# Optimization experiments

Hardware: AMD Instinct MI355X
Metric: run time of the kernel (lower is better)

## Reference

```python
import jax, jax.numpy as jnp
import numpy as np

D_MODEL = 1024
TEMPERATURE = 1.0

def setup_inputs() -> dict:
    key = jax.random.key(0)
    ks = jax.random.split(key, 9)
    B, NQ, NK, D = 4, 2048, 2048, D_MODEL
    s = 1.0 / np.sqrt(D)
    return {
        "Q": jax.random.normal(ks[0], (B, NQ, D), jnp.float32),
        "K": jax.random.normal(ks[1], (B, NK, D), jnp.float32),
        "V": jax.random.normal(ks[2], (B, NK, D), jnp.float32),
        "Wq": jax.random.normal(ks[3], (D, D), jnp.float32) * s,
        "bq": jax.random.normal(ks[4], (D,), jnp.float32) * 0.01,
        "Wk": jax.random.normal(ks[5], (D, D), jnp.float32) * s,
        "bk": jax.random.normal(ks[6], (D,), jnp.float32) * 0.01,
        "Wv": jax.random.normal(ks[7], (D, D), jnp.float32) * s,
        "bv": jax.random.normal(ks[8], (D,), jnp.float32) * 0.01,
    }

def reference(Q, K, V, Wq, bq, Wk, bk, Wv, bv):
    # torch nn.Linear: y = x @ W.T + b
    Qp = Q @ Wq.T + bq  # [B, NQ, D]
    Kp = K @ Wk.T + bk  # [B, NK, D]
    Vp = V @ Wv.T + bv  # [B, NK, D]

    # use_kl=True branch, vectorized:
    # kl[b,i,j] = D_KL(softmax(Kp[b,j]) || softmax(Qp[b,i]))
    #           = sum_d pK*(log pK - log pQ) = -H(pK_j) - pK_j . log pQ_i
    logpQ = jax.nn.log_softmax(Qp, axis=-1)  # [B, NQ, D]
    logpK = jax.nn.log_softmax(Kp, axis=-1)  # [B, NK, D]
    pK = jnp.exp(logpK)
    neg_ent_K = jnp.sum(pK * logpK, axis=-1)            # [B, NK], = -H(pK)
    cross = jnp.einsum('bjd,bid->bij', pK, logpQ)       # [B, NQ, NK]
    kl = neg_ent_K[:, None, :] - cross                  # [B, NQ, NK]
    scores = -kl / TEMPERATURE

    attn = jax.nn.softmax(scores, axis=-1)              # [B, NQ, NK]
    out = jnp.einsum('bij,bjd->bid', attn, Vp)          # [B, NQ, D]
    return out, attn
```

## Files before the change

### kernel.cpp

```cpp
#include <hip/hip_runtime.h>
#include <math.h>

#define D_MODEL 1024
#define NQS 2048
#define NKS 2048
#define BATCH 4

typedef __attribute__((ext_vector_type(8))) short bf16x8;
typedef __attribute__((ext_vector_type(4))) float f32x4;

#define AS1 __attribute__((address_space(1)))
#define AS3 __attribute__((address_space(3)))

__device__ __forceinline__ unsigned short f2bf(float f) {
  unsigned u = __builtin_bit_cast(unsigned, f);
  u = (u + 0x7FFF + ((u >> 16) & 1)) >> 16;
  return (unsigned short)u;
}
__device__ __forceinline__ float bf2f(unsigned short s) {
  return __builtin_bit_cast(float, ((unsigned)s) << 16);
}

__global__ __launch_bounds__(256) void cvt_k(const float* __restrict__ src,
                                             short* __restrict__ dst, int n8)
{
  int i = blockIdx.x * 256 + threadIdx.x;
  if (i >= n8) return;
  const float4 a = *(const float4*)&src[(long)i * 8];
  const float4 b = *(const float4*)&src[(long)i * 8 + 4];
  bf16x8 o;
  o[0] = (short)f2bf(a.x); o[1] = (short)f2bf(a.y);
  o[2] = (short)f2bf(a.z); o[3] = (short)f2bf(a.w);
  o[4] = (short)f2bf(b.x); o[5] = (short)f2bf(b.y);
  o[6] = (short)f2bf(b.z); o[7] = (short)f2bf(b.w);
  *(bf16x8*)&dst[(long)i * 8] = o;
}

__global__ __launch_bounds__(256, 2) void mfma_abt_k(
    const short* __restrict__ A, const short* __restrict__ B,
    const float* __restrict__ bias, float bscale,
    float* __restrict__ Cf, short* __restrict__ Cbf,
    int N, int K, long sA, long sB, long sC, long sBias)
{
  __shared__ short As[128 * 32];
  __shared__ short Bs[128 * 32];
  const int bz = blockIdx.z;
  const short* Ab = A + (long)bz * sA;
  const short* Bb = B + (long)bz * sB;
  const int gm = blockIdx.y * 128, gn = blockIdx.x * 128;
  const int t = threadIdx.x;
  const int lane = t & 63, w = t >> 6;
  const int wm = w >> 1, wn = w & 1;

  const int srow = lane >> 2, sq = lane & 3;
  const short* ga0 = Ab + (long)(gm + w * 32 + srow) * K + sq * 8;
  const short* ga1 = Ab + (long)(gm + w * 32 + 16 + srow) * K + sq * 8;
  const short* gb0 = Bb + (long)(gn + w * 32 + srow) * K + sq * 8;
  const short* gb1 = Bb + (long)(gn + w * 32 + 16 + srow) * K + sq * 8;
  short* la0 = As + (w * 2 + 0) * 512;
  short* la1 = As + (w * 2 + 1) * 512;
  short* lb0 = Bs + (w * 2 + 0) * 512;
  short* lb1 = Bs + (w * 2 + 1) * 512;

  const int frow = lane & 15, fq = lane >> 4;

  f32x4 acc[4][4] = {};

  for (int k0 = 0; k0 < K; k0 += 32) {
    __builtin_amdgcn_global_load_lds((const AS1 void*)(ga0 + k0),
                                     (AS3 void*)la0, 16, 0, 0);
    __builtin_amdgcn_global_load_lds((const AS1 void*)(ga1 + k0),
                                     (AS3 void*)la1, 16, 0, 0);
    __builtin_amdgcn_global_load_lds((const AS1 void*)(gb0 + k0),
                                     (AS3 void*)lb0, 16, 0, 0);
    __builtin_amdgcn_global_load_lds((const AS1 void*)(gb1 + k0),
                                     (AS3 void*)lb1, 16, 0, 0);
    __syncthreads();
    bf16x8 af[4], bfm[4];
#pragma unroll
    for (int mi = 0; mi < 4; ++mi)
      af[mi] = *(const bf16x8*)&As[(wm * 64 + mi * 16 + frow) * 32 + fq * 8];
#pragma unroll
    for (int ni = 0; ni < 4; ++ni)
      bfm[ni] = *(const bf16x8*)&Bs[(wn * 64 + ni * 16 + frow) * 32 + fq * 8];
#pragma unroll
    for (int mi = 0; mi < 4; ++mi)
#pragma unroll
      for (int ni = 0; ni < 4; ++ni)
        acc[mi][ni] = __builtin_amdgcn_mfma_f32_16x16x32_bf16(
            af[mi], bfm[ni], acc[mi][ni], 0, 0, 0);
    __syncthreads();
  }

  float bb[4];
#pragma unroll
  for (int ni = 0; ni < 4; ++ni)
    bb[ni] = bias ? bias[(long)bz * sBias + gn + wn * 64 + ni * 16 + frow] * bscale
                  : 0.f;

#pragma unroll
  for (int mi = 0; mi < 4; ++mi) {
#pragma unroll
    for (int r = 0; r < 4; ++r) {
      const long row = gm + wm * 64 + mi * 16 + fq * 4 + r;
#pragma unroll
      for (int ni = 0; ni < 4; ++ni) {
        const long col = gn + wn * 64 + ni * 16 + frow;
        float v = acc[mi][ni][r] + bb[ni];
        if (Cf) Cf[(long)bz * sC + row * N + col] = v;
        else    Cbf[(long)bz * sC + row * N + col] = (short)f2bf(v);
      }
    }
  }
}

__global__ __launch_bounds__(256) void kstats_k(short* __restrict__ KP,
                                                float* __restrict__ negent)
{
  __shared__ float red[4];
  const long row = blockIdx.x;
  short* x = KP + row * (long)D_MODEL;
  const int t = threadIdx.x;
  short4 raw = *(const short4*)&x[t * 4];
  float v0 = bf2f((unsigned short)raw.x), v1 = bf2f((unsigned short)raw.y);
  float v2 = bf2f((unsigned short)raw.z), v3 = bf2f((unsigned short)raw.w);
  float m = fmaxf(fmaxf(v0, v1), fmaxf(v2, v3));
  for (int o = 32; o; o >>= 1) m = fmaxf(m, __shfl_xor(m, o));
  if ((t & 63) == 0) red[t >> 6] = m;
  __syncthreads();
  m = fmaxf(fmaxf(red[0], red[1]), fmaxf(red[2], red[3]));
  __syncthreads();
  float e0 = expf(v0 - m), e1 = expf(v1 - m), e2 = expf(v2 - m),
        e3 = expf(v3 - m);
  float s = e0 + e1 + e2 + e3;
  for (int o = 32; o; o >>= 1) s += __shfl_xor(s, o);
  if ((t & 63) == 0) red[t >> 6] = s;
  __syncthreads();
  s = red[0] + red[1] + red[2] + red[3];
  __syncthreads();
  const float inv = 1.0f / s;
  const float lse = m + logf(s);
  float p0 = e0 * inv, p1 = e1 * inv, p2 = e2 * inv, p3 = e3 * inv;
  float ne = p0 * (v0 - lse) + p1 * (v1 - lse) + p2 * (v2 - lse) +
             p3 * (v3 - lse);
  for (int o = 32; o; o >>= 1) ne += __shfl_xor(ne, o);
  if ((t & 63) == 0) red[t >> 6] = ne;
  __syncthreads();
  if (t == 0) negent[row] = red[0] + red[1] + red[2] + red[3];
  short4 pw;
  pw.x = (short)f2bf(p0); pw.y = (short)f2bf(p1);
  pw.z = (short)f2bf(p2); pw.w = (short)f2bf(p3);
  *(short4*)&x[t * 4] = pw;
}

__global__ __launch_bounds__(256) void asoftmax_k(float* __restrict__ S,
                                                  short* __restrict__ Sbf)
{
  __shared__ float red[4];
  const long row = blockIdx.x;
  float* x = S + row * (long)NKS;
  short* y = Sbf + row * (long)NKS;
  const int t = threadIdx.x;
  float4 v0 = *(const float4*)&x[t * 4];
  float4 v1 = *(const float4*)&x[1024 + t * 4];
  float m = fmaxf(fmaxf(fmaxf(v0.x, v0.y), fmaxf(v0.z, v0.w)),
                  fmaxf(fmaxf(v1.x, v1.y), fmaxf(v1.z, v1.w)));
  for (int o = 32; o; o >>= 1) m = fmaxf(m, __shfl_xor(m, o));
  if ((t & 63) == 0) red[t >> 6] = m;
  __syncthreads();
  m = fmaxf(fmaxf(red[0], red[1]), fmaxf(red[2], red[3]));
  __syncthreads();
  float4 e0 = {expf(v0.x - m), expf(v0.y - m), expf(v0.z - m), expf(v0.w - m)};
  float4 e1 = {expf(v1.x - m), expf(v1.y - m), expf(v1.z - m), expf(v1.w - m)};
  float s = e0.x + e0.y + e0.z + e0.w + e1.x + e1.y + e1.z + e1.w;
  for (int o = 32; o; o >>= 1) s += __shfl_xor(s, o);
  if ((t & 63) == 0) red[t >> 6] = s;
  __syncthreads();
  s = red[0] + red[1] + red[2] + red[3];
  const float inv = 1.0f / s;
  float4 p0 = {e0.x * inv, e0.y * inv, e0.z * inv, e0.w * inv};
  float4 p1 = {e1.x * inv, e1.y * inv, e1.z * inv, e1.w * inv};
  *(float4*)&x[t * 4] = p0;
  *(float4*)&x[1024 + t * 4] = p1;
  short4 b0, b1;
  b0.x = (short)f2bf(p0.x); b0.y = (short)f2bf(p0.y);
  b0.z = (short)f2bf(p0.z); b0.w = (short)f2bf(p0.w);
  b1.x = (short)f2bf(p1.x); b1.y = (short)f2bf(p1.y);
  b1.z = (short)f2bf(p1.z); b1.w = (short)f2bf(p1.w);
  *(short4*)&y[t * 4] = b0;
  *(short4*)&y[1024 + t * 4] = b1;
}

__global__ __launch_bounds__(256) void transpose_k(const short* __restrict__ src,
                                                   short* __restrict__ dst)
{
  __shared__ short tile[64][68];
  const int j0 = blockIdx.x * 64;
  const int d0 = blockIdx.y * 64;
  const int t = threadIdx.x;
  const int r = t >> 2, c = t & 3;
#pragma unroll
  for (int i = 0; i < 4; ++i)
    *(short4*)&tile[r][c * 16 + i * 4] =
        *(const short4*)&src[(long)(j0 + r) * D_MODEL + d0 + c * 16 + i * 4];
  __syncthreads();
  const long b = j0 >> 11;
  const int jj = j0 & 2047;
#pragma unroll
  for (int i = 0; i < 4; ++i) {
    short4 o;
    o.x = tile[c * 16 + i * 4 + 0][r];
    o.y = tile[c * 16 + i * 4 + 1][r];
    o.z = tile[c * 16 + i * 4 + 2][r];
    o.w = tile[c * 16 + i * 4 + 3][r];
    *(short4*)&dst[b * ((long)D_MODEL * NKS) + (long)(d0 + r) * NKS + jj +
                   c * 16 + i * 4] = o;
  }
}

extern "C" void kernel_launch(void* const* d_in, const int* in_sizes, int n_in,
                              void* d_out, int out_size, void* d_ws,
                              size_t ws_size, hipStream_t stream)
{
  const float* Q = (const float*)d_in[0];
  const float* K = (const float*)d_in[1];
  const float* V = (const float*)d_in[2];
  const float* Wq = (const float*)d_in[3];
  const float* bq = (const float*)d_in[4];
  const float* Wk = (const float*)d_in[5];
  const float* bk = (const float*)d_in[6];
  const float* Wv = (const float*)d_in[7];
  const float* bv = (const float*)d_in[8];

  float* out = (float*)d_out;
  float* attn = out + (long)BATCH * NQS * D_MODEL;

  const long SZ = (long)BATCH * NQS * D_MODEL;
  short* ws = (short*)d_ws;
  short* Qbf = ws;
  short* Kbf = ws + SZ;
  short* Vbf = ws + 2 * SZ;
  short* Qp  = ws + 3 * SZ;
  short* pK  = ws + 4 * SZ;
  short* Vp  = ws + 5 * SZ;
  float* negent = (float*)(ws + 6 * SZ);
  short* attn_bf = ws;
  short* Vpt = ws + 2 * SZ;

  short* Wqb = (short*)attn;
  short* Wkb = Wqb + (long)D_MODEL * D_MODEL;
  short* Wvb = Wkb + (long)D_MODEL * D_MODEL;

  dim3 blk(256);
  const int n8x = (int)(SZ / 8);
  const int n8w = D_MODEL * D_MODEL / 8;

  cvt_k<<<dim3(n8x / 256), blk, 0, stream>>>(Q, Qbf, n8x);
  cvt_k<<<dim3(n8x / 256), blk, 0, stream>>>(K, Kbf, n8x);
  cvt_k<<<dim3(n8x / 256), blk, 0, stream>>>(V, Vbf, n8x);
  cvt_k<<<dim3(n8w / 256), blk, 0, stream>>>(Wq, Wqb, n8w);
  cvt_k<<<dim3(n8w / 256), blk, 0, stream>>>(Wk, Wkb, n8w);
  cvt_k<<<dim3(n8w / 256), blk, 0, stream>>>(Wv, Wvb, n8w);

  dim3 gp(D_MODEL / 128, (BATCH * NQS) / 128, 1);
  mfma_abt_k<<<gp, blk, 0, stream>>>(Qbf, Wqb, bq, 1.0f, nullptr, Qp,
                                     D_MODEL, D_MODEL, 0, 0, 0, 0);
  mfma_abt_k<<<gp, blk, 0, stream>>>(Kbf, Wkb, bk, 1.0f, nullptr, pK,
                                     D_MODEL, D_MODEL, 0, 0, 0, 0);
  mfma_abt_k<<<gp, blk, 0, stream>>>(Vbf, Wvb, bv, 1.0f, nullptr, Vp,
                                     D_MODEL, D_MODEL, 0, 0, 0, 0);

  kstats_k<<<dim3(BATCH * NKS), blk, 0, stream>>>(pK, negent);

  transpose_k<<<dim3((BATCH * NKS) / 64, D_MODEL / 64), blk, 0, stream>>>(Vp,
                                                                          Vpt);

  dim3 gs(NKS / 128, NQS / 128, BATCH);
  mfma_abt_k<<<gs, blk, 0, stream>>>(
      Qp, pK, negent, -1.0f, attn, nullptr, NKS, D_MODEL,
      (long)NQS * D_MODEL, (long)NKS * D_MODEL, (long)NQS * NKS, NKS);

  asoftmax_k<<<dim3(BATCH * NQS), blk, 0, stream>>>(attn, attn_bf);

  dim3 go(D_MODEL / 128, NQS / 128, BATCH);
  mfma_abt_k<<<go, blk, 0, stream>>>(
      attn_bf, Vpt, nullptr, 0.f, out, nullptr, D_MODEL, NKS,
      (long)NQS * NKS, (long)D_MODEL * NKS, (long)NQS * D_MODEL, 0);
}
```

Measured before the change: 430.8 us.

## Batch conversions and QKV projections into grouped launches, raise occupancy, use fast exp

```diff
diff --git a/kernel.cpp b/kernel.cpp
--- a/kernel.cpp
+++ b/kernel.cpp
@@ -21,9 +21,14 @@
   return __builtin_bit_cast(float, ((unsigned)s) << 16);
 }
 
-__global__ __launch_bounds__(256) void cvt_k(const float* __restrict__ src,
-                                             short* __restrict__ dst, int n8)
-{
+__global__ __launch_bounds__(256) void cvt3_k(
+    const float* __restrict__ s0, const float* __restrict__ s1,
+    const float* __restrict__ s2, short* __restrict__ d0,
+    short* __restrict__ d1, short* __restrict__ d2, int n8)
+{
+  const int z = blockIdx.z;
+  const float* src = z == 0 ? s0 : (z == 1 ? s1 : s2);
+  short* dst = z == 0 ? d0 : (z == 1 ? d1 : d2);
   int i = blockIdx.x * 256 + threadIdx.x;
   if (i >= n8) return;
   const float4 a = *(const float4*)&src[(long)i * 8];
@@ -36,17 +41,13 @@
   *(bf16x8*)&dst[(long)i * 8] = o;
 }
 
-__global__ __launch_bounds__(256, 2) void mfma_abt_k(
-    const short* __restrict__ A, const short* __restrict__ B,
-    const float* __restrict__ bias, float bscale,
-    float* __restrict__ Cf, short* __restrict__ Cbf,
-    int N, int K, long sA, long sB, long sC, long sBias)
+__device__ __forceinline__ void gemm_tile_body(
+    const short* __restrict__ Ab, const short* __restrict__ Bb,
+    const float* __restrict__ bias, float bscale, float* __restrict__ Cf,
+    short* __restrict__ Cbf, int N, int K)
 {
   __shared__ short As[128 * 32];
   __shared__ short Bs[128 * 32];
-  const int bz = blockIdx.z;
-  const short* Ab = A + (long)bz * sA;
-  const short* Bb = B + (long)bz * sB;
   const int gm = blockIdx.y * 128, gn = blockIdx.x * 128;
   const int t = threadIdx.x;
   const int lane = t & 63, w = t >> 6;
@@ -95,8 +96,7 @@
   float bb[4];
 #pragma unroll
   for (int ni = 0; ni < 4; ++ni)
-    bb[ni] = bias ? bias[(long)bz * sBias + gn + wn * 64 + ni * 16 + frow] * bscale
-                  : 0.f;
+    bb[ni] = bias ? bias[gn + wn * 64 + ni * 16 + frow] * bscale : 0.f;
 
 #pragma unroll
   for (int mi = 0; mi < 4; ++mi) {
@@ -107,11 +107,40 @@
       for (int ni = 0; ni < 4; ++ni) {
         const long col = gn + wn * 64 + ni * 16 + frow;
         float v = acc[mi][ni][r] + bb[ni];
-        if (Cf) Cf[(long)bz * sC + row * N + col] = v;
-        else    Cbf[(long)bz * sC + row * N + col] = (short)f2bf(v);
+        if (Cf) Cf[row * (long)N + col] = v;
+        else    Cbf[row * (long)N + col] = (short)f2bf(v);
       }
     }
   }
+}
+
+__global__ __launch_bounds__(256, 4) void mfma_abt_k(
+    const short* __restrict__ A, const short* __restrict__ B,
+    const float* __restrict__ bias, float bscale, float* __restrict__ Cf,
+    short* __restrict__ Cbf, int N, int K, long sA, long sB, long sC,
+    long sBias)
+{
+  const int bz = blockIdx.z;
+  gemm_tile_body(A + (long)bz * sA, B + (long)bz * sB,
+                 bias ? bias + (long)bz * sBias : nullptr, bscale,
+                 Cf ? Cf + (long)bz * sC : nullptr,
+                 Cbf ? Cbf + (long)bz * sC : nullptr, N, K);
+}
+
+__global__ __launch_bounds__(256, 4) void mfma_proj_k(
+    const short* __restrict__ Xq, const short* __restrict__ Xk,
+    const short* __restrict__ Xv, const short* __restrict__ Wq,
+    const short* __restrict__ Wk, const short* __restrict__ Wv,
+    const float* __restrict__ bq, const float* __restrict__ bk,
+    const float* __restrict__ bv, short* __restrict__ Oq,
+    short* __restrict__ Ok, short* __restrict__ Ov)
+{
+  const int z = blockIdx.z;
+  const short* X = z == 0 ? Xq : (z == 1 ? Xk : Xv);
+  const short* W = z == 0 ? Wq : (z == 1 ? Wk : Wv);
+  const float* bias = z == 0 ? bq : (z == 1 ? bk : bv);
+  short* O = z == 0 ? Oq : (z == 1 ? Ok : Ov);
+  gemm_tile_body(X, W, bias, 1.0f, nullptr, O, D_MODEL, D_MODEL);
 }
 
 __global__ __launch_bounds__(256) void kstats_k(short* __restrict__ KP,
@@ -130,8 +159,8 @@
   __syncthreads();
   m = fmaxf(fmaxf(red[0], red[1]), fmaxf(red[2], red[3]));
   __syncthreads();
-  float e0 = expf(v0 - m), e1 = expf(v1 - m), e2 = expf(v2 - m),
-        e3 = expf(v3 - m);
+  float e0 = __expf(v0 - m), e1 = __expf(v1 - m), e2 = __expf(v2 - m),
+        e3 = __expf(v3 - m);
   float s = e0 + e1 + e2 + e3;
   for (int o = 32; o; o >>= 1) s += __shfl_xor(s, o);
   if ((t & 63) == 0) red[t >> 6] = s;
@@ -139,7 +168,7 @@
   s = red[0] + red[1] + red[2] + red[3];
   __syncthreads();
   const float inv = 1.0f / s;
-  const float lse = m + logf(s);
+  const float lse = m + __logf(s);
   float p0 = e0 * inv, p1 = e1 * inv, p2 = e2 * inv, p3 = e3 * inv;
   float ne = p0 * (v0 - lse) + p1 * (v1 - lse) + p2 * (v2 - lse) +
              p3 * (v3 - lse);
@@ -170,8 +199,10 @@
   __syncthreads();
   m = fmaxf(fmaxf(red[0], red[1]), fmaxf(red[2], red[3]));
   __syncthreads();
-  float4 e0 = {expf(v0.x - m), expf(v0.y - m), expf(v0.z - m), expf(v0.w - m)};
-  float4 e1 = {expf(v1.x - m), expf(v1.y - m), expf(v1.z - m), expf(v1.w - m)};
+  float4 e0 = {__expf(v0.x - m), __expf(v0.y - m), __expf(v0.z - m),
+               __expf(v0.w - m)};
+  float4 e1 = {__expf(v1.x - m), __expf(v1.y - m), __expf(v1.z - m),
+               __expf(v1.w - m)};
   float s = e0.x + e0.y + e0.z + e0.w + e1.x + e1.y + e1.z + e1.w;
   for (int o = 32; o; o >>= 1) s += __shfl_xor(s, o);
   if ((t & 63) == 0) red[t >> 6] = s;
@@ -255,20 +286,14 @@
   const int n8x = (int)(SZ / 8);
   const int n8w = D_MODEL * D_MODEL / 8;
 
-  cvt_k<<<dim3(n8x / 256), blk, 0, stream>>>(Q, Qbf, n8x);
-  cvt_k<<<dim3(n8x / 256), blk, 0, stream>>>(K, Kbf, n8x);
-  cvt_k<<<dim3(n8x / 256), blk, 0, stream>>>(V, Vbf, n8x);
-  cvt_k<<<dim3(n8w / 256), blk, 0, stream>>>(Wq, Wqb, n8w);
-  cvt_k<<<dim3(n8w / 256), blk, 0, stream>>>(Wk, Wkb, n8w);
-  cvt_k<<<dim3(n8w / 256), blk, 0, stream>>>(Wv, Wvb, n8w);
-
-  dim3 gp(D_MODEL / 128, (BATCH * NQS) / 128, 1);
-  mfma_abt_k<<<gp, blk, 0, stream>>>(Qbf, Wqb, bq, 1.0f, nullptr, Qp,
-                                     D_MODEL, D_MODEL, 0, 0, 0, 0);
-  mfma_abt_k<<<gp, blk, 0, stream>>>(Kbf, Wkb, bk, 1.0f, nullptr, pK,
-                                     D_MODEL, D_MODEL, 0, 0, 0, 0);
-  mfma_abt_k<<<gp, blk, 0, stream>>>(Vbf, Wvb, bv, 1.0f, nullptr, Vp,
-                                     D_MODEL, D_MODEL, 0, 0, 0, 0);
+  cvt3_k<<<dim3(n8x / 256, 1, 3), blk, 0, stream>>>(Q, K, V, Qbf, Kbf, Vbf,
+                                                    n8x);
+  cvt3_k<<<dim3(n8w / 256, 1, 3), blk, 0, stream>>>(Wq, Wk, Wv, Wqb, Wkb, Wvb,
+                                                    n8w);
+
+  dim3 gp(D_MODEL / 128, (BATCH * NQS) / 128, 3);
+  mfma_proj_k<<<gp, blk, 0, stream>>>(Qbf, Kbf, Vbf, Wqb, Wkb, Wvb, bq, bk,
+                                      bv, Qp, pK, Vp);
 
   kstats_k<<<dim3(BATCH * NKS), blk, 0, stream>>>(pK, negent);
 
```

Measured after the change: 405.0 us. 6.0% less time.
